# Optimization experiments

Measured on AMD Instinct MI355X. Metric: run time of the kernel, lower is better.

The kernel has to match this reference:

```python
import jax, jax.numpy as jnp
import numpy as np

D_CONV = 4
DT_RANK = 32
D_STATE = 16


def setup_inputs() -> dict:
    key = jax.random.key(0)
    ks = jax.random.split(key, 12)
    B, Lt, d_model, d_inner = 2, 512, 512, 1024
    mk = lambda k, shape, scale=0.02: jax.random.normal(k, shape, dtype=jnp.float32) * scale
    inp = {}
    inp['t0'] = jax.random.normal(ks[0], (B, Lt, d_model), dtype=jnp.float32)
    inp['t1'] = jax.random.normal(ks[1], (B, Lt, d_model), dtype=jnp.float32)
    inp['t2'] = jax.random.normal(ks[2], (B, Lt, d_model), dtype=jnp.float32)
    inp['t3'] = jax.random.normal(ks[3], (B, Lt, d_model), dtype=jnp.float32)
    inp['in_proj_w'] = mk(ks[4], (2 * d_inner, d_model))
    inp['conv_w'] = mk(ks[5], (d_inner, 1, D_CONV), 0.2)
    inp['conv_b'] = jnp.zeros((d_inner,), jnp.float32)
    inp['x_proj_w'] = mk(ks[6], (DT_RANK + 2 * D_STATE, d_inner))
    s = DT_RANK ** (-0.5)
    inp['dt_w'] = jax.random.uniform(ks[7], (d_inner, DT_RANK), minval=-s, maxval=s, dtype=jnp.float32)
    dt = jnp.exp(jax.random.uniform(ks[8], (d_inner,), dtype=jnp.float32) * (np.log(0.1) - np.log(0.001)) + np.log(0.001))
    dt = jnp.clip(dt, 1e-4)
    inp['dt_b'] = dt + jnp.log(-jnp.expm1(-dt))
    inp['A_log'] = jnp.log(jnp.tile(jnp.arange(1, D_STATE + 1, dtype=jnp.float32), (d_inner, 1)))
    inp['D_param'] = jnp.ones((d_inner,), jnp.float32)
    inp['out_proj_w'] = mk(ks[9], (d_model, d_inner))
    return inp


def reference(t0, t1, t2, t3, in_proj_w, conv_w, conv_b, x_proj_w, dt_w, dt_b, A_log, D_param, out_proj_w):
    tensors = [t0, t1, t2, t3]
    # interleaved gather/concat: [B, 4*Lt, d_model]
    x = jnp.concatenate([t[:, i::4, :] for i in range(4) for t in tensors], axis=1)
    L = x.shape[1]
    xz = x @ in_proj_w.T                      # [B, L, 2*d_inner]
    xc, z = jnp.split(xz, 2, axis=-1)
    # causal depthwise conv1d (torch pads both sides K-1 then truncates to L == left pad only)
    xc = xc.transpose(0, 2, 1)                # [B, d_inner, L]
    xc = jax.lax.conv_general_dilated(
        xc, conv_w, window_strides=(1,), padding=[(D_CONV - 1, 0)],
        dimension_numbers=('NCH', 'OIH', 'NCH'), feature_group_count=xc.shape[1])
    xc = xc + conv_b[None, :, None]
    xc = jax.nn.silu(xc.transpose(0, 2, 1))   # [B, L, d_inner]
    # SSM
    A = -jnp.exp(A_log)                       # [d_inner, d_state]
    dbc = xc @ x_proj_w.T                     # [B, L, dt_rank + 2*d_state]
    delta, Bm, Cm = jnp.split(dbc, [DT_RANK, DT_RANK + D_STATE], axis=-1)
    delta = jax.nn.softplus(delta @ dt_w.T + dt_b)  # [B, L, d_inner]
    deltaA = jnp.exp(delta[..., None] * A)          # [B, L, d_inner, d_state]
    BX = (delta * xc)[..., None] * Bm[:, :, None, :]  # deltaB * x

    def op(c1, c2):
        a1, b1 = c1
        a2, b2 = c2
        return a1 * a2, a2 * b1 + b2

    _, hs = jax.lax.associative_scan(op, (deltaA, BX), axis=1)  # h_t = dA_t h_{t-1} + BX_t
    y = jnp.einsum('blds,bls->bld', hs, Cm) + D_param * xc
    out = (y * jax.nn.silu(z)) @ out_proj_w.T  # [B, L, d_model]
    Lt = L // 4
    return tuple(out[:, i::4, :][:, :Lt, :] + tensors[i] for i in range(4))
```

## Files before the change

### kernel.cpp

```cpp
#include <hip/hip_runtime.h>

#define NB 2
#define LT 512
#define LL 2048
#define MM 4096
#define DMODEL 512
#define DINNER 1024
#define DTRANK 32
#define DSTATE 16
#define NSEG 128
#define SEGLEN 16
#define NST (NB * DINNER * DSTATE)
#define NSCAN (NSEG * NB * DINNER)
#define KCH 8

typedef short bf16x8 __attribute__((ext_vector_type(8)));
typedef float f32x4  __attribute__((ext_vector_type(4)));

__device__ __forceinline__ float silu_f(float x) { return x / (1.f + __expf(-x)); }
__device__ __forceinline__ unsigned short f2b(float f) {
    unsigned u = __float_as_uint(f);
    u += 0x7fffu + ((u >> 16) & 1u);
    return (unsigned short)(u >> 16);
}
__device__ __forceinline__ float b2f(unsigned short u) {
    return __uint_as_float(((unsigned)u) << 16);
}

__global__ __launch_bounds__(256) void k_inproj(
    const float* __restrict__ t0, const float* __restrict__ t1,
    const float* __restrict__ t2, const float* __restrict__ t3,
    const float* __restrict__ W,
    float* __restrict__ xc_raw, unsigned short* __restrict__ zb)
{
    __shared__ short As[128 * 40];
    __shared__ short Bs[128 * 40];
    const int t = threadIdx.x;
    const int lane = t & 63;
    const int wid = t >> 6;
    const int wm = wid >> 1, wn = wid & 1;
    const int bm = blockIdx.x, bn = blockIdx.y;

    const int srow  = t >> 1;
    const int shalf = (t & 1) * 16;

    const int arow = bm * 128 + srow;
    const int gb = arow >> 11;
    const int gl = arow & 2047;
    const int gc = gl >> 7, gr = gl & 127;
    const int ti = gc & 3, ci = gc >> 2;
    const float* tp = (ti == 0) ? t0 : (ti == 1) ? t1 : (ti == 2) ? t2 : t3;
    const float* asrc = tp + ((size_t)gb * 512 + (size_t)(ci + 4 * gr)) * 512 + shalf;
    const float* bsrc = W + (size_t)(bn * 128 + srow) * 512 + shalf;

    f32x4 acc[4][4];
#pragma unroll
    for (int i = 0; i < 4; ++i)
#pragma unroll
        for (int j = 0; j < 4; ++j) acc[i][j] = (f32x4){0.f, 0.f, 0.f, 0.f};

    float4 ra[4], rb[4];
#pragma unroll
    for (int q = 0; q < 4; ++q) {
        ra[q] = *(const float4*)(asrc + q * 4);
        rb[q] = *(const float4*)(bsrc + q * 4);
    }

    const int ko = (lane >> 4) * 8;
    const int fr = lane & 15;

    for (int ks = 0; ks < 512 / 32; ++ks) {
        __syncthreads();
        {
            bf16x8 v0, v1, w0, w1;
            v0[0]=f2b(ra[0].x); v0[1]=f2b(ra[0].y); v0[2]=f2b(ra[0].z); v0[3]=f2b(ra[0].w);
            v0[4]=f2b(ra[1].x); v0[5]=f2b(ra[1].y); v0[6]=f2b(ra[1].z); v0[7]=f2b(ra[1].w);
            v1[0]=f2b(ra[2].x); v1[1]=f2b(ra[2].y); v1[2]=f2b(ra[2].z); v1[3]=f2b(ra[2].w);
            v1[4]=f2b(ra[3].x); v1[5]=f2b(ra[3].y); v1[6]=f2b(ra[3].z); v1[7]=f2b(ra[3].w);
            w0[0]=f2b(rb[0].x); w0[1]=f2b(rb[0].y); w0[2]=f2b(rb[0].z); w0[3]=f2b(rb[0].w);
            w0[4]=f2b(rb[1].x); w0[5]=f2b(rb[1].y); w0[6]=f2b(rb[1].z); w0[7]=f2b(rb[1].w);
            w1[0]=f2b(rb[2].x); w1[1]=f2b(rb[2].y); w1[2]=f2b(rb[2].z); w1[3]=f2b(rb[2].w);
            w1[4]=f2b(rb[3].x); w1[5]=f2b(rb[3].y); w1[6]=f2b(rb[3].z); w1[7]=f2b(rb[3].w);
            *(bf16x8*)&As[srow * 40 + shalf]     = v0;
            *(bf16x8*)&As[srow * 40 + shalf + 8] = v1;
            *(bf16x8*)&Bs[srow * 40 + shalf]     = w0;
            *(bf16x8*)&Bs[srow * 40 + shalf + 8] = w1;
        }
        __syncthreads();
        if (ks + 1 < 512 / 32) {
            const int k0 = (ks + 1) * 32;
#pragma unroll
            for (int q = 0; q < 4; ++q) {
                ra[q] = *(const float4*)(asrc + k0 + q * 4);
                rb[q] = *(const float4*)(bsrc + k0 + q * 4);
            }
        }
        bf16x8 af[4], bfr[4];
#pragma unroll
        for (int mf = 0; mf < 4; ++mf)
            af[mf] = *(const bf16x8*)&As[(wm * 64 + mf * 16 + fr) * 40 + ko];
#pragma unroll
        for (int nf = 0; nf < 4; ++nf)
            bfr[nf] = *(const bf16x8*)&Bs[(wn * 64 + nf * 16 + fr) * 40 + ko];
#pragma unroll
        for (int mf = 0; mf < 4; ++mf)
#pragma unroll
            for (int nf = 0; nf < 4; ++nf)
                acc[mf][nf] = __builtin_amdgcn_mfma_f32_16x16x32_bf16(
                    af[mf], bfr[nf], acc[mf][nf], 0, 0, 0);
    }

    if (bn < 8) {
#pragma unroll
        for (int mf = 0; mf < 4; ++mf) {
            const int gmb = bm * 128 + wm * 64 + mf * 16 + (lane >> 4) * 4;
#pragma unroll
            for (int nf = 0; nf < 4; ++nf) {
                const int gn = bn * 128 + wn * 64 + nf * 16 + (lane & 15);
#pragma unroll
                for (int j = 0; j < 4; ++j)
                    xc_raw[(size_t)(gmb + j) * DINNER + gn] = acc[mf][nf][j];
            }
        }
    } else {
#pragma unroll
        for (int mf = 0; mf < 4; ++mf) {
            const int gmb = bm * 128 + wm * 64 + mf * 16 + (lane >> 4) * 4;
#pragma unroll
            for (int nf = 0; nf < 4; ++nf) {
                const int gn = bn * 128 + wn * 64 + nf * 16 + (lane & 15) - 1024;
#pragma unroll
                for (int j = 0; j < 4; ++j)
                    zb[(size_t)(gmb + j) * DINNER + gn] = f2b(acc[mf][nf][j]);
            }
        }
    }
}

__global__ __launch_bounds__(256) void k_conv(
    const float* __restrict__ xc_raw, const float* __restrict__ cw,
    const float* __restrict__ cb, const unsigned short* __restrict__ zb,
    unsigned short* __restrict__ xc_b, unsigned int* __restrict__ xzp_t)
{
    const int d  = blockIdx.y * 256 + threadIdx.x;
    const int mt = blockIdx.x;
    const int m0 = mt * 16;
    const int l0 = m0 & 2047;

    float w[4];
#pragma unroll
    for (int k = 0; k < 4; ++k) w[k] = cw[(size_t)d * 4 + k];
    const float bias = cb[d];

    float r[19];
#pragma unroll
    for (int o = 0; o < 19; ++o) {
        const int l = l0 + o - 3;
        r[o] = (l >= 0) ? xc_raw[(size_t)(m0 + o - 3) * DINNER + d] : 0.f;
    }

    unsigned uu[16];
#pragma unroll
    for (int mm = 0; mm < 16; ++mm) {
        float s = bias;
#pragma unroll
        for (int k = 0; k < 4; ++k) s += w[k] * r[mm + k];
        const unsigned short x16 = f2b(silu_f(s));
        const unsigned short z16 = zb[(size_t)(m0 + mm) * DINNER + d];
        xc_b[(size_t)(m0 + mm) * DINNER + d] = x16;
        uu[mm] = ((unsigned)z16 << 16) | (unsigned)x16;
    }
    unsigned int* dst = xzp_t + ((size_t)mt * DINNER + d) * 16;
    *(uint4*)(dst + 0)  = *(const uint4*)&uu[0];
    *(uint4*)(dst + 4)  = *(const uint4*)&uu[4];
    *(uint4*)(dst + 8)  = *(const uint4*)&uu[8];
    *(uint4*)(dst + 12) = *(const uint4*)&uu[12];
}

__global__ __launch_bounds__(256) void k_cvt_wx(
    const float* __restrict__ Wx, unsigned short* __restrict__ wxb)
{
    const int i4 = blockIdx.x * 256 + threadIdx.x;
    float4 v = *(const float4*)(Wx + (size_t)i4 * 4);
    ushort4 o;
    o.x = f2b(v.x); o.y = f2b(v.y); o.z = f2b(v.z); o.w = f2b(v.w);
    *(ushort4*)(wxb + (size_t)i4 * 4) = o;
}

__global__ __launch_bounds__(256) void k_xproj_mfma(
    const unsigned short* __restrict__ xc_b, const unsigned short* __restrict__ wxb,
    float* __restrict__ part)
{
    __shared__ short As[128 * 136];
    __shared__ short Bs[64 * 136];
    const int t = threadIdx.x;
    const int lane = t & 63;
    const int w = t >> 6;
    const int bm = blockIdx.x;
    const int kc = blockIdx.y;

    {
        const int row = t >> 1;
        const int cb0 = (t & 1) * 64;
        const unsigned short* src = xc_b + (size_t)(bm * 128 + row) * 1024 + kc * 128 + cb0;
#pragma unroll
        for (int q = 0; q < 8; ++q)
            *(bf16x8*)&As[row * 136 + cb0 + q * 8] = *(const bf16x8*)(src + q * 8);
    }
    {
        const int row = t >> 2;
        const int cb0 = (t & 3) * 32;
        const unsigned short* src = wxb + (size_t)row * 1024 + kc * 128 + cb0;
#pragma unroll
        for (int q = 0; q < 4; ++q)
            *(bf16x8*)&Bs[row * 136 + cb0 + q * 8] = *(const bf16x8*)(src + q * 8);
    }
    __syncthreads();

    const int fr = lane & 15;
    const int ko = (lane >> 4) * 8;

    f32x4 acc[2][4];
#pragma unroll
    for (int i = 0; i < 2; ++i)
#pragma unroll
        for (int j = 0; j < 4; ++j) acc[i][j] = (f32x4){0.f, 0.f, 0.f, 0.f};

#pragma unroll
    for (int ks = 0; ks < 4; ++ks) {
        const int kb = ks * 32 + ko;
        bf16x8 af[2], bfr[4];
#pragma unroll
        for (int mf = 0; mf < 2; ++mf)
            af[mf] = *(const bf16x8*)&As[(w * 32 + mf * 16 + fr) * 136 + kb];
#pragma unroll
        for (int nf = 0; nf < 4; ++nf)
            bfr[nf] = *(const bf16x8*)&Bs[(nf * 16 + fr) * 136 + kb];
#pragma unroll
        for (int mf = 0; mf < 2; ++mf)
#pragma unroll
            for (int nf = 0; nf < 4; ++nf)
                acc[mf][nf] = __builtin_amdgcn_mfma_f32_16x16x32_bf16(
                    af[mf], bfr[nf], acc[mf][nf], 0, 0, 0);
    }

    float* pb = part + (size_t)kc * (MM * 64);
#pragma unroll
    for (int mf = 0; mf < 2; ++mf) {
        const int rb = bm * 128 + w * 32 + mf * 16 + (lane >> 4) * 4;
#pragma unroll
        for (int nf = 0; nf < 4; ++nf) {
            const int col = nf * 16 + (lane & 15);
#pragma unroll
            for (int j = 0; j < 4; ++j)
                pb[(size_t)(rb + j) * 64 + col] = acc[mf][nf][j];
        }
    }
}

__global__ __launch_bounds__(256) void k_xreduce(
    const float* __restrict__ part, float* __restrict__ dbc)
{
    const int i = blockIdx.x * 256 + threadIdx.x;
    float s = 0.f;
#pragma unroll
    for (int kc = 0; kc < KCH; ++kc)
        s += part[(size_t)kc * (MM * 64) + i];
    dbc[i] = s;
}

__global__ __launch_bounds__(256) void k_dtproj(
    const float* __restrict__ dbc, const float* __restrict__ dtw,
    const float* __restrict__ dtb, const unsigned short* __restrict__ xc_b,
    unsigned int* __restrict__ dxp_t)
{
    const int tid = threadIdx.x;
    const int mt = blockIdx.x;
    const int m0 = mt * 16;
    const int d  = blockIdx.y * 256 + tid;

    float w[DTRANK];
#pragma unroll
    for (int q = 0; q < 8; ++q) {
        float4 v = *(const float4*)(dtw + (size_t)d * DTRANK + q * 4);
        w[q * 4 + 0] = v.x; w[q * 4 + 1] = v.y;
        w[q * 4 + 2] = v.z; w[q * 4 + 3] = v.w;
    }
    const float bias = dtb[d];

    unsigned uu[16];
#pragma unroll
    for (int m = 0; m < 16; ++m) {
        const float* bc = dbc + (size_t)(m0 + m) * 64;
        float s0 = bias, s1 = 0.f, s2 = 0.f, s3 = 0.f;
#pragma unroll
        for (int r = 0; r < DTRANK; r += 4) {
            s0 += bc[r + 0] * w[r + 0];
            s1 += bc[r + 1] * w[r + 1];
            s2 += bc[r + 2] * w[r + 2];
            s3 += bc[r + 3] * w[r + 3];
        }
        const float s = (s0 + s1) + (s2 + s3);
        const float sp = (s > 20.f) ? s : __logf(1.f + __expf(s));
        const float xv = b2f(xc_b[(size_t)(m0 + m) * DINNER + d]);
        uu[m] = ((unsigned)f2b(sp * xv) << 16) | (unsigned)f2b(sp);
    }
    unsigned int* dst = dxp_t + ((size_t)mt * DINNER + d) * 16;
    *(uint4*)(dst + 0)  = *(const uint4*)&uu[0];
    *(uint4*)(dst + 4)  = *(const uint4*)&uu[4];
    *(uint4*)(dst + 8)  = *(const uint4*)&uu[8];
    *(uint4*)(dst + 12) = *(const uint4*)&uu[12];
}

__global__ __launch_bounds__(256) void k_scan_partial(
    const unsigned int* __restrict__ dxp_t, const float* __restrict__ dbc,
    const float* __restrict__ A_log,
    float* __restrict__ hfin, float* __restrict__ aprod)
{
    const int gid = blockIdx.x * 256 + threadIdx.x;
    const int d = gid & 1023;
    const int b = (gid >> 10) & (NB - 1);
    const int g = gid >> 11;

    float Af[DSTATE];
#pragma unroll
    for (int q = 0; q < 4; ++q) {
        float4 a4 = *(const float4*)(A_log + d * DSTATE + q * 4);
        Af[q * 4 + 0] = -__expf(a4.x);
        Af[q * 4 + 1] = -__expf(a4.y);
        Af[q * 4 + 2] = -__expf(a4.z);
        Af[q * 4 + 3] = -__expf(a4.w);
    }

    const int mtile = b * 128 + g;
    unsigned uu[16];
    {
        const unsigned int* src = dxp_t + ((size_t)mtile * DINNER + d) * 16;
        *(uint4*)&uu[0]  = *(const uint4*)(src + 0);
        *(uint4*)&uu[4]  = *(const uint4*)(src + 4);
        *(uint4*)&uu[8]  = *(const uint4*)(src + 8);
        *(uint4*)&uu[12] = *(const uint4*)(src + 12);
    }

    float h[DSTATE], ap[DSTATE];
#pragma unroll
    for (int s = 0; s < DSTATE; ++s) { h[s] = 0.f; ap[s] = 1.f; }

    const int mbase = b * LL + g * SEGLEN;

    float Bv[DSTATE];
    {
        const int mu = __builtin_amdgcn_readfirstlane(mbase);
        const float* bc = dbc + (size_t)mu * 64 + 32;
#pragma unroll
        for (int q = 0; q < 4; ++q) {
            float4 b4 = *(const float4*)(bc + q * 4);
            Bv[q * 4 + 0] = b4.x; Bv[q * 4 + 1] = b4.y;
            Bv[q * 4 + 2] = b4.z; Bv[q * 4 + 3] = b4.w;
        }
    }

#pragma unroll
    for (int ll = 0; ll < SEGLEN; ++ll) {
        float Bn[DSTATE];
        if (ll + 1 < SEGLEN) {
            const int mun = __builtin_amdgcn_readfirstlane(mbase + ll + 1);
            const float* bcn = dbc + (size_t)mun * 64 + 32;
#pragma unroll
            for (int q = 0; q < 4; ++q) {
                float4 b4 = *(const float4*)(bcn + q * 4);
                Bn[q * 4 + 0] = b4.x; Bn[q * 4 + 1] = b4.y;
                Bn[q * 4 + 2] = b4.z; Bn[q * 4 + 3] = b4.w;
            }
        }
        const float de = __uint_as_float(uu[ll] << 16);
        const float dx = __uint_as_float(uu[ll] & 0xFFFF0000u);
#pragma unroll
        for (int s = 0; s < DSTATE; ++s) {
            const float dA = __expf(de * Af[s]);
            ap[s] *= dA;
            h[s] = dA * h[s] + dx * Bv[s];
        }
        if (ll + 1 < SEGLEN) {
#pragma unroll
            for (int s = 0; s < DSTATE; ++s) Bv[s] = Bn[s];
        }
    }

    const size_t base = ((size_t)(b * DINNER + d) * NSEG + g) * 16;
    *(float4*)&hfin [base + 0]  = *(const float4*)&h[0];
    *(float4*)&hfin [base + 4]  = *(const float4*)&h[4];
    *(float4*)&hfin [base + 8]  = *(const float4*)&h[8];
    *(float4*)&hfin [base + 12] = *(const float4*)&h[12];
    *(float4*)&aprod[base + 0]  = *(const float4*)&ap[0];
    *(float4*)&aprod[base + 4]  = *(const float4*)&ap[4];
    *(float4*)&aprod[base + 8]  = *(const float4*)&ap[8];
    *(float4*)&aprod[base + 12] = *(const float4*)&ap[12];
}

__global__ __launch_bounds__(256) void k_scan_combine(
    float* __restrict__ hfin, const float* __restrict__ aprod)
{
    const int tid = blockIdx.x * 256 + threadIdx.x;
    const int g = tid & 63;
    const size_t bd = (size_t)(tid >> 6);
    const size_t base = (bd * NSEG + 2 * g) * 16;

    float A0[16], B0[16], A1[16], B1[16];
#pragma unroll
    for (int q = 0; q < 4; ++q) {
        *(float4*)&A0[q * 4] = *(const float4*)&aprod[base + q * 4];
        *(float4*)&B0[q * 4] = *(const float4*)&hfin [base + q * 4];
        *(float4*)&A1[q * 4] = *(const float4*)&aprod[base + 16 + q * 4];
        *(float4*)&B1[q * 4] = *(const float4*)&hfin [base + 16 + q * 4];
    }

    float A[16], B[16];
#pragma unroll
    for (int s = 0; s < 16; ++s) {
        A[s] = A1[s] * A0[s];
        B[s] = A1[s] * B0[s] + B1[s];
    }
#pragma unroll
    for (int off = 1; off < 64; off <<= 1) {
#pragma unroll
        for (int s = 0; s < 16; ++s) {
            const float Ap = __shfl_up(A[s], off, 64);
            const float Bp = __shfl_up(B[s], off, 64);
            if (g >= off) { B[s] = A[s] * Bp + B[s]; A[s] = A[s] * Ap; }
        }
    }
    float E[16], E1[16];
#pragma unroll
    for (int s = 0; s < 16; ++s) {
        float e = __shfl_up(B[s], 1, 64);
        if (g == 0) e = 0.f;
        E[s] = e;
        E1[s] = A0[s] * e + B0[s];
    }
#pragma unroll
    for (int q = 0; q < 4; ++q) {
        *(float4*)&hfin[base + q * 4]      = *(const float4*)&E[q * 4];
        *(float4*)&hfin[base + 16 + q * 4] = *(const float4*)&E1[q * 4];
    }
}

__global__ __launch_bounds__(256) void k_scan_final(
    const unsigned int* __restrict__ dxp_t, const unsigned int* __restrict__ xzp_t,
    const float* __restrict__ dbc, const float* __restrict__ A_log,
    const float* __restrict__ Dp, const float* __restrict__ hin,
    unsigned short* __restrict__ yzb)
{
    const int gid = blockIdx.x * 256 + threadIdx.x;
    const int d = gid & 1023;
    const int b = (gid >> 10) & (NB - 1);
    const int g = gid >> 11;

    float Af[DSTATE];
#pragma unroll
    for (int q = 0; q < 4; ++q) {
        float4 a4 = *(const float4*)(A_log + d * DSTATE + q * 4);
        Af[q * 4 + 0] = -__expf(a4.x);
        Af[q * 4 + 1] = -__expf(a4.y);
        Af[q * 4 + 2] = -__expf(a4.z);
        Af[q * 4 + 3] = -__expf(a4.w);
    }
    const float Dd = Dp[d];

    const int mtile = b * 128 + g;
    unsigned uu[16], vv[16];
    {
        const unsigned int* su = dxp_t + ((size_t)mtile * DINNER + d) * 16;
        const unsigned int* sv = xzp_t + ((size_t)mtile * DINNER + d) * 16;
#pragma unroll
        for (int q = 0; q < 4; ++q) {
            *(uint4*)&uu[q * 4] = *(const uint4*)(su + q * 4);
            *(uint4*)&vv[q * 4] = *(const uint4*)(sv + q * 4);
        }
    }

    float h[DSTATE];
    {
        const size_t base = ((size_t)(b * DINNER + d) * NSEG + g) * 16;
#pragma unroll
        for (int q = 0; q < 4; ++q)
            *(float4*)&h[q * 4] = *(const float4*)&hin[base + q * 4];
    }

    const int mbase = b * LL + g * SEGLEN;

    float Bv[DSTATE], Cv[DSTATE];
    {
        const int mu = __builtin_amdgcn_readfirstlane(mbase);
        const float* bc = dbc + (size_t)mu * 64;
#pragma unroll
        for (int q = 0; q < 4; ++q) {
            float4 b4 = *(const float4*)(bc + 32 + q * 4);
            float4 c4 = *(const float4*)(bc + 48 + q * 4);
            Bv[q * 4 + 0] = b4.x; Bv[q * 4 + 1] = b4.y;
            Bv[q * 4 + 2] = b4.z; Bv[q * 4 + 3] = b4.w;
            Cv[q * 4 + 0] = c4.x; Cv[q * 4 + 1] = c4.y;
            Cv[q * 4 + 2] = c4.z; Cv[q * 4 + 3] = c4.w;
        }
    }

#pragma unroll
    for (int ll = 0; ll < SEGLEN; ++ll) {
        float Bn[DSTATE], Cn[DSTATE];
        if (ll + 1 < SEGLEN) {
            const int mun = __builtin_amdgcn_readfirstlane(mbase + ll + 1);
            const float* bcn = dbc + (size_t)mun * 64;
#pragma unroll
            for (int q = 0; q < 4; ++q) {
                float4 b4 = *(const float4*)(bcn + 32 + q * 4);
                float4 c4 = *(const float4*)(bcn + 48 + q * 4);
                Bn[q * 4 + 0] = b4.x; Bn[q * 4 + 1] = b4.y;
                Bn[q * 4 + 2] = b4.z; Bn[q * 4 + 3] = b4.w;
                Cn[q * 4 + 0] = c4.x; Cn[q * 4 + 1] = c4.y;
                Cn[q * 4 + 2] = c4.z; Cn[q * 4 + 3] = c4.w;
            }
        }
        const float de = __uint_as_float(uu[ll] << 16);
        const float dx = __uint_as_float(uu[ll] & 0xFFFF0000u);
        const float x  = __uint_as_float(vv[ll] << 16);
        const float zz = __uint_as_float(vv[ll] & 0xFFFF0000u);
        float y0 = 0.f, y1 = 0.f, y2 = 0.f, y3 = 0.f;
#pragma unroll
        for (int s = 0; s < DSTATE; s += 4) {
            float dA;
            dA = __expf(de * Af[s + 0]); h[s + 0] = dA * h[s + 0] + dx * Bv[s + 0]; y0 += h[s + 0] * Cv[s + 0];
            dA = __expf(de * Af[s + 1]); h[s + 1] = dA * h[s + 1] + dx * Bv[s + 1]; y1 += h[s + 1] * Cv[s + 1];
            dA = __expf(de * Af[s + 2]); h[s + 2] = dA * h[s + 2] + dx * Bv[s + 2]; y2 += h[s + 2] * Cv[s + 2];
            dA = __expf(de * Af[s + 3]); h[s + 3] = dA * h[s + 3] + dx * Bv[s + 3]; y3 += h[s + 3] * Cv[s + 3];
        }
        const float y = (y0 + y1) + (y2 + y3);
        yzb[(size_t)(mbase + ll) * DINNER + d] = f2b((y + Dd * x) * silu_f(zz));
        if (ll + 1 < SEGLEN) {
#pragma unroll
            for (int s = 0; s < DSTATE; ++s) { Bv[s] = Bn[s]; Cv[s] = Cn[s]; }
        }
    }
}

__global__ __launch_bounds__(256) void k_outproj(
    const unsigned short* __restrict__ yzb, const float* __restrict__ Wo,
    const float* __restrict__ t0, const float* __restrict__ t1,
    const float* __restrict__ t2, const float* __restrict__ t3,
    float* __restrict__ outp)
{
    __shared__ short As[64 * 40];
    __shared__ short Bs[64 * 40];
    const int t = threadIdx.x;
    const int lane = t & 63;
    const int wid = t >> 6;
    const int wm = wid >> 1, wn = wid & 1;
    const int bm = blockIdx.x;
    const int bn = blockIdx.y;

    const int srow = t >> 2;
    const int scol = (t & 3) * 8;

    const unsigned short* asrc = yzb + (size_t)(bm * 64 + srow) * DINNER + scol;
    const float* bsrc = Wo + (size_t)(bn * 64 + srow) * DINNER + scol;

    f32x4 acc[2][2];
#pragma unroll
    for (int i = 0; i < 2; ++i)
#pragma unroll
        for (int j = 0; j < 2; ++j) acc[i][j] = (f32x4){0.f, 0.f, 0.f, 0.f};

    bf16x8 raA = *(const bf16x8*)asrc;
    float4 rb[2];
#pragma unroll
    for (int q = 0; q < 2; ++q) rb[q] = *(const float4*)(bsrc + q * 4);

    const int ko = (lane >> 4) * 8;
    const int fr = lane & 15;

    for (int ks = 0; ks < DINNER / 32; ++ks) {
        __syncthreads();
        {
            bf16x8 w0;
            w0[0]=f2b(rb[0].x); w0[1]=f2b(rb[0].y); w0[2]=f2b(rb[0].z); w0[3]=f2b(rb[0].w);
            w0[4]=f2b(rb[1].x); w0[5]=f2b(rb[1].y); w0[6]=f2b(rb[1].z); w0[7]=f2b(rb[1].w);
            *(bf16x8*)&As[srow * 40 + scol] = raA;
            *(bf16x8*)&Bs[srow * 40 + scol] = w0;
        }
        __syncthreads();
        if (ks + 1 < DINNER / 32) {
            const int k0 = (ks + 1) * 32;
            raA = *(const bf16x8*)(asrc + k0);
#pragma unroll
            for (int q = 0; q < 2; ++q) rb[q] = *(const float4*)(bsrc + k0 + q * 4);
        }
        bf16x8 af[2], bfr[2];
#pragma unroll
        for (int mf = 0; mf < 2; ++mf)
            af[mf] = *(const bf16x8*)&As[(wm * 32 + mf * 16 + fr) * 40 + ko];
#pragma unroll
        for (int nf = 0; nf < 2; ++nf)
            bfr[nf] = *(const bf16x8*)&Bs[(wn * 32 + nf * 16 + fr) * 40 + ko];
#pragma unroll
        for (int mf = 0; mf < 2; ++mf)
#pragma unroll
            for (int nf = 0; nf < 2; ++nf)
                acc[mf][nf] = __builtin_amdgcn_mfma_f32_16x16x32_bf16(
                    af[mf], bfr[nf], acc[mf][nf], 0, 0, 0);
    }

#pragma unroll
    for (int mf = 0; mf < 2; ++mf) {
#pragma unroll
        for (int j = 0; j < 4; ++j) {
            const int gm = bm * 64 + wm * 32 + mf * 16 + (lane >> 4) * 4 + j;
            const int b = gm >> 11;
            const int l = gm & 2047;
            const int ii = l & 3;
            const int jj = l >> 2;
            const float* tsel = (ii == 0) ? t0 : (ii == 1) ? t1 : (ii == 2) ? t2 : t3;
#pragma unroll
            for (int nf = 0; nf < 2; ++nf) {
                const int gn = bn * 64 + wn * 32 + nf * 16 + (lane & 15);
                const float tv = tsel[((size_t)b * 512 + jj) * 512 + gn];
                outp[(((size_t)ii * NB + b) * 512 + jj) * 512 + gn] = acc[mf][nf][j] + tv;
            }
        }
    }
}

extern "C" void kernel_launch(void* const* d_in, const int* in_sizes, int n_in,
                              void* d_out, int out_size, void* d_ws, size_t ws_size,
                              hipStream_t stream)
{
    const float* t0 = (const float*)d_in[0];
    const float* t1 = (const float*)d_in[1];
    const float* t2 = (const float*)d_in[2];
    const float* t3 = (const float*)d_in[3];
    const float* in_proj_w  = (const float*)d_in[4];
    const float* conv_w     = (const float*)d_in[5];
    const float* conv_b     = (const float*)d_in[6];
    const float* x_proj_w   = (const float*)d_in[7];
    const float* dt_w       = (const float*)d_in[8];
    const float* dt_b       = (const float*)d_in[9];
    const float* A_log      = (const float*)d_in[10];
    const float* D_param    = (const float*)d_in[11];
    const float* out_proj_w = (const float*)d_in[12];
    float* outp = (float*)d_out;

    float* xc_raw = (float*)d_ws;
    unsigned short* xc_b = (unsigned short*)(xc_raw + (size_t)MM * DINNER);
    unsigned int* dxp_t = (unsigned int*)(xc_b + (size_t)MM * DINNER);
    unsigned int* xzp_t = dxp_t + (size_t)MM * DINNER;
    float* dbc  = (float*)(xzp_t + (size_t)MM * DINNER);
    float* hfin = dbc + (size_t)MM * 64;
    float* part  = xc_raw;
    unsigned short* wxb = (unsigned short*)(xc_raw + (size_t)KCH * MM * 64);
    float* aprod = xc_raw;
    unsigned short* yzb = (unsigned short*)xc_raw;
    unsigned short* zb  = (unsigned short*)hfin;

    k_inproj<<<dim3(32, 16), 256, 0, stream>>>(t0, t1, t2, t3, in_proj_w, xc_raw, zb);
    k_conv<<<dim3(MM / 16, 4), 256, 0, stream>>>(xc_raw, conv_w, conv_b, zb, xc_b, xzp_t);
    k_cvt_wx<<<64, 256, 0, stream>>>(x_proj_w, wxb);
    k_xproj_mfma<<<dim3(32, KCH), 256, 0, stream>>>(xc_b, wxb, part);
    k_xreduce<<<(MM * 64) / 256, 256, 0, stream>>>(part, dbc);
    k_dtproj<<<dim3(MM / 16, 4), 256, 0, stream>>>(dbc, dt_w, dt_b, xc_b, dxp_t);
    k_scan_partial<<<NSCAN / 256, 256, 0, stream>>>(dxp_t, dbc, A_log, hfin, aprod);
    k_scan_combine<<<(NB * DINNER * 64) / 256, 256, 0, stream>>>(hfin, aprod);
    k_scan_final<<<NSCAN / 256, 256, 0, stream>>>(dxp_t, xzp_t, dbc, A_log, D_param, hfin, yzb);
    k_outproj<<<dim3(64, 8), 256, 0, stream>>>(yzb, out_proj_w, t0, t1, t2, t3, outp);
}
```

Before: 154.3 us.

## Store packed dt/x and x/z buffers in row-major token-by-channel layout

The packed delta/deltaX and x/z buffers move from a per-16-token tile-transposed layout to plain [token][channel] row-major. Producers (conv, dtproj) and consumers (scan_partial, scan_final) now write and read one 32-bit word per token, so adjacent threads (adjacent channels) touch consecutive addresses. The previous layout used 64-byte per-thread uint4 stores and loads with a 64-byte stride between lanes. The aim is better coalescing across the wavefront, in exchange for more, smaller memory instructions; dtproj's loop is also only partially unrolled now.

```diff
diff --git a/kernel.cpp b/kernel.cpp
--- a/kernel.cpp
+++ b/kernel.cpp
@@ -140,7 +140,7 @@
 __global__ __launch_bounds__(256) void k_conv(
     const float* __restrict__ xc_raw, const float* __restrict__ cw,
     const float* __restrict__ cb, const unsigned short* __restrict__ zb,
-    unsigned short* __restrict__ xc_b, unsigned int* __restrict__ xzp_t)
+    unsigned short* __restrict__ xc_b, unsigned int* __restrict__ xzp)
 {
     const int d  = blockIdx.y * 256 + threadIdx.x;
     const int mt = blockIdx.x;
@@ -159,22 +159,17 @@
         r[o] = (l >= 0) ? xc_raw[(size_t)(m0 + o - 3) * DINNER + d] : 0.f;
     }
 
-    unsigned uu[16];
 #pragma unroll
     for (int mm = 0; mm < 16; ++mm) {
         float s = bias;
 #pragma unroll
         for (int k = 0; k < 4; ++k) s += w[k] * r[mm + k];
         const unsigned short x16 = f2b(silu_f(s));
-        const unsigned short z16 = zb[(size_t)(m0 + mm) * DINNER + d];
-        xc_b[(size_t)(m0 + mm) * DINNER + d] = x16;
-        uu[mm] = ((unsigned)z16 << 16) | (unsigned)x16;
-    }
-    unsigned int* dst = xzp_t + ((size_t)mt * DINNER + d) * 16;
-    *(uint4*)(dst + 0)  = *(const uint4*)&uu[0];
-    *(uint4*)(dst + 4)  = *(const uint4*)&uu[4];
-    *(uint4*)(dst + 8)  = *(const uint4*)&uu[8];
-    *(uint4*)(dst + 12) = *(const uint4*)&uu[12];
+        const size_t idx = (size_t)(m0 + mm) * DINNER + d;
+        const unsigned short z16 = zb[idx];
+        xc_b[idx] = x16;
+        xzp[idx] = ((unsigned)z16 << 16) | (unsigned)x16;
+    }
 }
 
 __global__ __launch_bounds__(256) void k_cvt_wx(
@@ -272,11 +267,10 @@
 __global__ __launch_bounds__(256) void k_dtproj(
     const float* __restrict__ dbc, const float* __restrict__ dtw,
     const float* __restrict__ dtb, const unsigned short* __restrict__ xc_b,
-    unsigned int* __restrict__ dxp_t)
+    unsigned int* __restrict__ dxp)
 {
     const int tid = threadIdx.x;
-    const int mt = blockIdx.x;
-    const int m0 = mt * 16;
+    const int m0 = blockIdx.x * 16;
     const int d  = blockIdx.y * 256 + tid;
 
     float w[DTRANK];
@@ -288,8 +282,7 @@
     }
     const float bias = dtb[d];
 
-    unsigned uu[16];
-#pragma unroll
+#pragma unroll 4
     for (int m = 0; m < 16; ++m) {
         const float* bc = dbc + (size_t)(m0 + m) * 64;
         float s0 = bias, s1 = 0.f, s2 = 0.f, s3 = 0.f;
@@ -302,18 +295,14 @@
         }
         const float s = (s0 + s1) + (s2 + s3);
         const float sp = (s > 20.f) ? s : __logf(1.f + __expf(s));
-        const float xv = b2f(xc_b[(size_t)(m0 + m) * DINNER + d]);
-        uu[m] = ((unsigned)f2b(sp * xv) << 16) | (unsigned)f2b(sp);
-    }
-    unsigned int* dst = dxp_t + ((size_t)mt * DINNER + d) * 16;
-    *(uint4*)(dst + 0)  = *(const uint4*)&uu[0];
-    *(uint4*)(dst + 4)  = *(const uint4*)&uu[4];
-    *(uint4*)(dst + 8)  = *(const uint4*)&uu[8];
-    *(uint4*)(dst + 12) = *(const uint4*)&uu[12];
+        const size_t idx = (size_t)(m0 + m) * DINNER + d;
+        const float xv = b2f(xc_b[idx]);
+        dxp[idx] = ((unsigned)f2b(sp * xv) << 16) | (unsigned)f2b(sp);
+    }
 }
 
 __global__ __launch_bounds__(256) void k_scan_partial(
-    const unsigned int* __restrict__ dxp_t, const float* __restrict__ dbc,
+    const unsigned int* __restrict__ dxp, const float* __restrict__ dbc,
     const float* __restrict__ A_log,
     float* __restrict__ hfin, float* __restrict__ aprod)
 {
@@ -332,21 +321,15 @@
         Af[q * 4 + 3] = -__expf(a4.w);
     }
 
-    const int mtile = b * 128 + g;
+    const int mbase = b * LL + g * SEGLEN;
     unsigned uu[16];
-    {
-        const unsigned int* src = dxp_t + ((size_t)mtile * DINNER + d) * 16;
-        *(uint4*)&uu[0]  = *(const uint4*)(src + 0);
-        *(uint4*)&uu[4]  = *(const uint4*)(src + 4);
-        *(uint4*)&uu[8]  = *(const uint4*)(src + 8);
-        *(uint4*)&uu[12] = *(const uint4*)(src + 12);
-    }
+#pragma unroll
+    for (int m = 0; m < 16; ++m)
+        uu[m] = dxp[(size_t)(mbase + m) * DINNER + d];
 
     float h[DSTATE], ap[DSTATE];
 #pragma unroll
     for (int s = 0; s < DSTATE; ++s) { h[s] = 0.f; ap[s] = 1.f; }
-
-    const int mbase = b * LL + g * SEGLEN;
 
     float Bv[DSTATE];
     {
@@ -446,7 +429,7 @@
 }
 
 __global__ __launch_bounds__(256) void k_scan_final(
-    const unsigned int* __restrict__ dxp_t, const unsigned int* __restrict__ xzp_t,
+    const unsigned int* __restrict__ dxp, const unsigned int* __restrict__ xzp,
     const float* __restrict__ dbc, const float* __restrict__ A_log,
     const float* __restrict__ Dp, const float* __restrict__ hin,
     unsigned short* __restrict__ yzb)
@@ -467,16 +450,12 @@
     }
     const float Dd = Dp[d];
 
-    const int mtile = b * 128 + g;
+    const int mbase = b * LL + g * SEGLEN;
     unsigned uu[16], vv[16];
-    {
-        const unsigned int* su = dxp_t + ((size_t)mtile * DINNER + d) * 16;
-        const unsigned int* sv = xzp_t + ((size_t)mtile * DINNER + d) * 16;
-#pragma unroll
-        for (int q = 0; q < 4; ++q) {
-            *(uint4*)&uu[q * 4] = *(const uint4*)(su + q * 4);
-            *(uint4*)&vv[q * 4] = *(const uint4*)(sv + q * 4);
-        }
+#pragma unroll
+    for (int m = 0; m < 16; ++m) {
+        uu[m] = dxp[(size_t)(mbase + m) * DINNER + d];
+        vv[m] = xzp[(size_t)(mbase + m) * DINNER + d];
     }
 
     float h[DSTATE];
@@ -486,8 +465,6 @@
         for (int q = 0; q < 4; ++q)
             *(float4*)&h[q * 4] = *(const float4*)&hin[base + q * 4];
     }
-
-    const int mbase = b * LL + g * SEGLEN;
 
     float Bv[DSTATE], Cv[DSTATE];
     {
@@ -649,9 +626,9 @@
 
     float* xc_raw = (float*)d_ws;
     unsigned short* xc_b = (unsigned short*)(xc_raw + (size_t)MM * DINNER);
-    unsigned int* dxp_t = (unsigned int*)(xc_b + (size_t)MM * DINNER);
-    unsigned int* xzp_t = dxp_t + (size_t)MM * DINNER;
-    float* dbc  = (float*)(xzp_t + (size_t)MM * DINNER);
+    unsigned int* dxp = (unsigned int*)(xc_b + (size_t)MM * DINNER);
+    unsigned int* xzp = dxp + (size_t)MM * DINNER;
+    float* dbc  = (float*)(xzp + (size_t)MM * DINNER);
     float* hfin = dbc + (size_t)MM * 64;
     float* part  = xc_raw;
     unsigned short* wxb = (unsigned short*)(xc_raw + (size_t)KCH * MM * 64);
@@ -660,13 +637,13 @@
     unsigned short* zb  = (unsigned short*)hfin;
 
     k_inproj<<<dim3(32, 16), 256, 0, stream>>>(t0, t1, t2, t3, in_proj_w, xc_raw, zb);
-    k_conv<<<dim3(MM / 16, 4), 256, 0, stream>>>(xc_raw, conv_w, conv_b, zb, xc_b, xzp_t);
+    k_conv<<<dim3(MM / 16, 4), 256, 0, stream>>>(xc_raw, conv_w, conv_b, zb, xc_b, xzp);
     k_cvt_wx<<<64, 256, 0, stream>>>(x_proj_w, wxb);
     k_xproj_mfma<<<dim3(32, KCH), 256, 0, stream>>>(xc_b, wxb, part);
     k_xreduce<<<(MM * 64) / 256, 256, 0, stream>>>(part, dbc);
-    k_dtproj<<<dim3(MM / 16, 4), 256, 0, stream>>>(dbc, dt_w, dt_b, xc_b, dxp_t);
-    k_scan_partial<<<NSCAN / 256, 256, 0, stream>>>(dxp_t, dbc, A_log, hfin, aprod);
+    k_dtproj<<<dim3(MM / 16, 4), 256, 0, stream>>>(dbc, dt_w, dt_b, xc_b, dxp);
+    k_scan_partial<<<NSCAN / 256, 256, 0, stream>>>(dxp, dbc, A_log, hfin, aprod);
     k_scan_combine<<<(NB * DINNER * 64) / 256, 256, 0, stream>>>(hfin, aprod);
-    k_scan_final<<<NSCAN / 256, 256, 0, stream>>>(dxp_t, xzp_t, dbc, A_log, D_param, hfin, yzb);
+    k_scan_final<<<NSCAN / 256, 256, 0, stream>>>(dxp, xzp, dbc, A_log, D_param, hfin, yzb);
     k_outproj<<<dim3(64, 8), 256, 0, stream>>>(yzb, out_proj_w, t0, t1, t2, t3, outp);
 }
```

Result: faster. 146.6 us (-5.0%).
